# Kernel tuning notes

Hardware: AMD Instinct MI355X
Metric: run time of the kernel (lower is better)

## Reference

```python
import jax, jax.numpy as jnp
import numpy as np


def setup_inputs() -> dict:
    key = jax.random.key(0)
    k1, k2, k3 = jax.random.split(key, 3)
    b, n, h, d = 2, 2048, 16, 64
    q = jax.random.normal(k1, (b, n, h, d), dtype=jnp.float32)
    k = jax.random.normal(k2, (b, n, h, d), dtype=jnp.float32)
    v = jax.random.normal(k3, (b, n, h, d), dtype=jnp.float32)
    return {"q": q, "k": k, "v": v, "is_causal": 1}


def reference(q, k, v, is_causal):
    # q, k, v: [b, n, h, d]
    b, n, h, d = q.shape
    scale = 1.0 / jnp.sqrt(jnp.asarray(d, dtype=q.dtype))
    # scores: [b, h, n_q, n_k]
    scores = jnp.einsum("bqhd,bkhd->bhqk", q, k) * scale
    if is_causal:
        causal_mask = jnp.triu(jnp.ones((n, n), dtype=bool), k=1)  # True above diagonal
        scores = jnp.where(causal_mask[None, None, :, :], jnp.asarray(-jnp.inf, scores.dtype), scores)
    attn = jax.nn.softmax(scores, axis=-1)
    # output back to [b, n, h, d]
    out = jnp.einsum("bhqk,bkhd->bqhd", attn, v)
    return out
```

## Files before the change

kernel.cpp:

```cpp
#include <hip/hip_runtime.h>
#include <hip/hip_bf16.h>
#include <math.h>

typedef __bf16 bf16x8 __attribute__((ext_vector_type(8)));
typedef __bf16 bf16x4 __attribute__((ext_vector_type(4)));
typedef float  f32x4  __attribute__((ext_vector_type(4)));

#define HD  64
#define NQT 32
#define LDK 72
#define LDV 68
#define LDP 72

__global__ __launch_bounds__(256, 4)
void fattn_fwd(const float* __restrict__ Q, const float* __restrict__ K,
               const float* __restrict__ V, const int* __restrict__ causal_p,
               float* __restrict__ O, int B, int N, int H) {
  __shared__ alignas(16) __bf16 Kl[64][LDK];
  __shared__ alignas(16) __bf16 Vl[64][LDV];
  __shared__ alignas(16) __bf16 Pl[64][LDP];

  const int tid  = threadIdx.x;
  const int wave = tid >> 6;
  const int lane = tid & 63;
  const int lo = lane & 15, hi = lane >> 4;

  const int x  = (NQT - 1) - (blockIdx.x >> 5);
  const int bh = blockIdx.x & 31;
  const int bb = bh / H, hh = bh - bb * H;

  const int causal = causal_p[0];
  const int sN = H * HD;

  const float* Qb = Q + (long)bb * N * sN + hh * HD;
  const float* Kb = K + (long)bb * N * sN + hh * HD;
  const float* Vb = V + (long)bb * N * sN + hh * HD;
  float*       Ob = O + (long)bb * N * sN + hh * HD;

  const int q0 = x * 64;
  const int ntile = causal ? (x + 1) : NQT;

  const float qscale = 0.125f * 1.44269504088896340736f;
  bf16x8 aq[2];
  {
    const float* qp = Qb + (long)(q0 + wave * 16 + lo) * sN;
#pragma unroll
    for (int c = 0; c < 2; ++c) {
      f32x4 x0 = *(const f32x4*)(qp + c * 32 + hi * 8);
      f32x4 x1 = *(const f32x4*)(qp + c * 32 + hi * 8 + 4);
      bf16x8 a;
#pragma unroll
      for (int j = 0; j < 4; ++j) {
        a[j]     = (__bf16)(x0[j] * qscale);
        a[j + 4] = (__bf16)(x1[j] * qscale);
      }
      aq[c] = a;
    }
  }

  f32x4 acc[4];
  float m_run[4], l_run[4];
#pragma unroll
  for (int i = 0; i < 4; ++i) {
    acc[i] = (f32x4){0.f, 0.f, 0.f, 0.f};
    m_run[i] = -INFINITY;
    l_run[i] = 0.f;
  }

  f32x4 kreg[4], vreg[4];
  auto issue = [&](int tt) {
    const int k0 = tt * 64;
#pragma unroll
    for (int i = 0; i < 4; ++i) {
      const int fl = tid + i * 256;
      const int r = fl >> 4, c4 = (fl & 15) * 4;
      kreg[i] = *(const f32x4*)(Kb + (long)(k0 + r) * sN + c4);
    }
    const float* vrow = Vb + (long)(k0 + wave * 16 + hi * 4) * sN + lo * 4;
#pragma unroll
    for (int q = 0; q < 4; ++q) vreg[q] = *(const f32x4*)(vrow + (long)q * sN);
  };
  auto wr = [&]() {
#pragma unroll
    for (int i = 0; i < 4; ++i) {
      const int fl = tid + i * 256;
      const int r = fl >> 4, c4 = (fl & 15) * 4;
      bf16x4 kb;
#pragma unroll
      for (int j = 0; j < 4; ++j) kb[j] = (__bf16)kreg[i][j];
      *(bf16x4*)&Kl[r][c4] = kb;
    }
#pragma unroll
    for (int j = 0; j < 4; ++j) {
      bf16x4 vv;
#pragma unroll
      for (int q = 0; q < 4; ++q) vv[q] = (__bf16)vreg[q][j];
      *(bf16x4*)&Vl[lo * 4 + j][wave * 16 + hi * 4] = vv;
    }
  };

  issue(0);
  wr();
  __syncthreads();

  for (int t = 0; t < ntile; ++t) {
    const bool pf = (t + 1 < ntile);
    if (pf) issue(t + 1);
    const int k0 = t * 64;

    f32x4 s[4];
#pragma unroll
    for (int nt = 0; nt < 4; ++nt) s[nt] = (f32x4){0.f, 0.f, 0.f, 0.f};
#pragma unroll
    for (int c = 0; c < 2; ++c) {
#pragma unroll
      for (int nt = 0; nt < 4; ++nt) {
        bf16x8 b = *(const bf16x8*)&Kl[nt * 16 + lo][c * 32 + hi * 8];
        s[nt] = __builtin_amdgcn_mfma_f32_16x16x32_bf16(aq[c], b, s[nt], 0, 0, 0);
      }
    }

    if (causal && t == x) {
#pragma unroll
      for (int nt = 0; nt < 4; ++nt) {
        const int kvg = k0 + nt * 16 + lo;
#pragma unroll
        for (int r = 0; r < 4; ++r) {
          const int qg = q0 + wave * 16 + hi * 4 + r;
          if (kvg > qg) s[nt][r] = -INFINITY;
        }
      }
    }

#pragma unroll
    for (int r = 0; r < 4; ++r) {
      float mx = fmaxf(fmaxf(s[0][r], s[1][r]), fmaxf(s[2][r], s[3][r]));
      mx = fmaxf(mx, __shfl_xor(mx, 1));
      mx = fmaxf(mx, __shfl_xor(mx, 2));
      mx = fmaxf(mx, __shfl_xor(mx, 4));
      mx = fmaxf(mx, __shfl_xor(mx, 8));
      const float mnew = fmaxf(m_run[r], mx);
      const float fac  = exp2f(m_run[r] - mnew);
      float ps = 0.f;
#pragma unroll
      for (int nt = 0; nt < 4; ++nt) {
        const float p = exp2f(s[nt][r] - mnew);
        s[nt][r] = p;
        ps += p;
      }
      ps += __shfl_xor(ps, 1);
      ps += __shfl_xor(ps, 2);
      ps += __shfl_xor(ps, 4);
      ps += __shfl_xor(ps, 8);
      l_run[r] = l_run[r] * fac + ps;
      m_run[r] = mnew;
#pragma unroll
      for (int nt = 0; nt < 4; ++nt) acc[nt][r] *= fac;
    }

    asm volatile("s_waitcnt lgkmcnt(0)" ::: "memory");
#pragma unroll
    for (int nt = 0; nt < 4; ++nt)
#pragma unroll
      for (int r = 0; r < 4; ++r)
        Pl[wave * 16 + hi * 4 + r][nt * 16 + lo] = (__bf16)s[nt][r];
    asm volatile("s_waitcnt lgkmcnt(0)" ::: "memory");

#pragma unroll
    for (int c = 0; c < 2; ++c) {
      bf16x8 pa = *(const bf16x8*)&Pl[wave * 16 + lo][c * 32 + hi * 8];
#pragma unroll
      for (int nt = 0; nt < 4; ++nt) {
        const __bf16* vp = &Vl[nt * 16 + lo][c * 32 + hi * 8];
        bf16x4 v0 = *(const bf16x4*)vp;
        bf16x4 v1 = *(const bf16x4*)(vp + 4);
        bf16x8 vb;
#pragma unroll
        for (int j = 0; j < 4; ++j) { vb[j] = v0[j]; vb[j + 4] = v1[j]; }
        acc[nt] = __builtin_amdgcn_mfma_f32_16x16x32_bf16(pa, vb, acc[nt], 0, 0, 0);
      }
    }

    __syncthreads();
    if (pf) wr();
    __syncthreads();
  }

  {
    const int qrow = q0 + wave * 16 + hi * 4;
#pragma unroll
    for (int nt = 0; nt < 4; ++nt) {
#pragma unroll
      for (int r = 0; r < 4; ++r) {
        Ob[(long)(qrow + r) * sN + nt * 16 + lo] = acc[nt][r] / l_run[r];
      }
    }
  }
}

extern "C" void kernel_launch(void* const* d_in, const int* in_sizes, int n_in,
                              void* d_out, int out_size, void* d_ws, size_t ws_size,
                              hipStream_t stream) {
  const float* q = (const float*)d_in[0];
  const float* k = (const float*)d_in[1];
  const float* v = (const float*)d_in[2];
  const int* causal = (const int*)d_in[3];
  float* out = (float*)d_out;
  const int B = 2, N = 2048, H = 16;
  dim3 grid(NQT * B * H);
  fattn_fwd<<<grid, dim3(256), 0, stream>>>(q, k, v, causal, out, B, N, H);
}
```

Baseline: 159.7 us.

## Switch to 32x32 MFMA with register-resident P and swizzled LDS tiles

Moves to 128-query blocks where each wave owns 32 queries and uses 32x32x16 bf16 MFMAs with a transposed formulation (S^T = K·Q^T, O^T = V^T·P^T). The softmax probabilities are repacked in registers with cross-half shuffles instead of going through an LDS P buffer. K and V tiles are XOR-swizzled in LDS to avoid bank conflicts, and output stores are vectorised. The aim is to cut LDS traffic and synchronisation per tile and raise MFMA efficiency. The cost is higher register pressure (launch bounds drop to 2), half as many blocks, and coarser causal load balance.

```diff
diff --git a/kernel.cpp b/kernel.cpp
--- a/kernel.cpp
+++ b/kernel.cpp
@@ -4,28 +4,38 @@
 
 typedef __bf16 bf16x8 __attribute__((ext_vector_type(8)));
 typedef __bf16 bf16x4 __attribute__((ext_vector_type(4)));
+typedef __bf16 bf16x2 __attribute__((ext_vector_type(2)));
 typedef float  f32x4  __attribute__((ext_vector_type(4)));
-
-#define HD  64
-#define NQT 32
-#define LDK 72
-#define LDV 68
-#define LDP 72
-
-__global__ __launch_bounds__(256, 4)
+typedef float  f32x16 __attribute__((ext_vector_type(16)));
+typedef unsigned int u32;
+typedef unsigned int u32x4 __attribute__((ext_vector_type(4)));
+
+#define HD   64
+#define NQB  16
+#define MNEG (-1e30f)
+#define KSW(r, c) ((c) ^ (((r) & 7) << 3))
+#define VSW(r, c) ((c) ^ ((((r) >> 2) & 7) << 3))
+
+static __device__ __forceinline__ u32 pkbf(float a, float b) {
+  bf16x2 t; t[0] = (__bf16)a; t[1] = (__bf16)b;
+  return __builtin_bit_cast(u32, t);
+}
+
+__global__ __launch_bounds__(256, 2)
 void fattn_fwd(const float* __restrict__ Q, const float* __restrict__ K,
                const float* __restrict__ V, const int* __restrict__ causal_p,
                float* __restrict__ O, int B, int N, int H) {
-  __shared__ alignas(16) __bf16 Kl[64][LDK];
-  __shared__ alignas(16) __bf16 Vl[64][LDV];
-  __shared__ alignas(16) __bf16 Pl[64][LDP];
+  __shared__ alignas(16) __bf16 Kl[64][64];
+  __shared__ alignas(16) __bf16 Vt[64][64];
 
   const int tid  = threadIdx.x;
   const int wave = tid >> 6;
   const int lane = tid & 63;
-  const int lo = lane & 15, hi = lane >> 4;
-
-  const int x  = (NQT - 1) - (blockIdx.x >> 5);
+  const int l31  = lane & 31;
+  const int h    = lane >> 5;
+  const int lo16 = lane & 15, hi4 = lane >> 4;
+
+  const int x  = (NQB - 1) - ((int)blockIdx.x >> 5);
   const int bh = blockIdx.x & 31;
   const int bb = bh / H, hh = bh - bb * H;
 
@@ -37,35 +47,31 @@
   const float* Vb = V + (long)bb * N * sN + hh * HD;
   float*       Ob = O + (long)bb * N * sN + hh * HD;
 
-  const int q0 = x * 64;
-  const int ntile = causal ? (x + 1) : NQT;
+  const int q0w   = x * 128 + wave * 32;
+  const int ntile = causal ? (2 * x + 2) : (2 * NQB);
 
   const float qscale = 0.125f * 1.44269504088896340736f;
-  bf16x8 aq[2];
+  bf16x8 aq[4];
   {
-    const float* qp = Qb + (long)(q0 + wave * 16 + lo) * sN;
-#pragma unroll
-    for (int c = 0; c < 2; ++c) {
-      f32x4 x0 = *(const f32x4*)(qp + c * 32 + hi * 8);
-      f32x4 x1 = *(const f32x4*)(qp + c * 32 + hi * 8 + 4);
+    const float* qrow = Qb + (long)(q0w + l31) * sN;
+#pragma unroll
+    for (int ds = 0; ds < 4; ++ds) {
+      f32x4 x0 = *(const f32x4*)(qrow + ds * 16 + h * 8);
+      f32x4 x1 = *(const f32x4*)(qrow + ds * 16 + h * 8 + 4);
       bf16x8 a;
 #pragma unroll
       for (int j = 0; j < 4; ++j) {
         a[j]     = (__bf16)(x0[j] * qscale);
         a[j + 4] = (__bf16)(x1[j] * qscale);
       }
-      aq[c] = a;
+      aq[ds] = a;
     }
   }
 
-  f32x4 acc[4];
-  float m_run[4], l_run[4];
-#pragma unroll
-  for (int i = 0; i < 4; ++i) {
-    acc[i] = (f32x4){0.f, 0.f, 0.f, 0.f};
-    m_run[i] = -INFINITY;
-    l_run[i] = 0.f;
-  }
+  f32x16 accA, accB;
+#pragma unroll
+  for (int j = 0; j < 16; ++j) { accA[j] = 0.f; accB[j] = 0.f; }
+  float m_run = MNEG, l_run = 0.f;
 
   f32x4 kreg[4], vreg[4];
   auto issue = [&](int tt) {
@@ -76,7 +82,7 @@
       const int r = fl >> 4, c4 = (fl & 15) * 4;
       kreg[i] = *(const f32x4*)(Kb + (long)(k0 + r) * sN + c4);
     }
-    const float* vrow = Vb + (long)(k0 + wave * 16 + hi * 4) * sN + lo * 4;
+    const float* vrow = Vb + (long)(k0 + wave * 16 + hi4 * 4) * sN + lo16 * 4;
 #pragma unroll
     for (int q = 0; q < 4; ++q) vreg[q] = *(const f32x4*)(vrow + (long)q * sN);
   };
@@ -88,14 +94,16 @@
       bf16x4 kb;
 #pragma unroll
       for (int j = 0; j < 4; ++j) kb[j] = (__bf16)kreg[i][j];
-      *(bf16x4*)&Kl[r][c4] = kb;
-    }
+      *(bf16x4*)&Kl[r][KSW(r, c4)] = kb;
+    }
+    const int kv0 = wave * 16 + hi4 * 4;
 #pragma unroll
     for (int j = 0; j < 4; ++j) {
+      const int d = lo16 * 4 + j;
       bf16x4 vv;
 #pragma unroll
       for (int q = 0; q < 4; ++q) vv[q] = (__bf16)vreg[q][j];
-      *(bf16x4*)&Vl[lo * 4 + j][wave * 16 + hi * 4] = vv;
+      *(bf16x4*)&Vt[d][VSW(d, kv0)] = vv;
     }
   };
 
@@ -108,77 +116,92 @@
     if (pf) issue(t + 1);
     const int k0 = t * 64;
 
-    f32x4 s[4];
-#pragma unroll
-    for (int nt = 0; nt < 4; ++nt) s[nt] = (f32x4){0.f, 0.f, 0.f, 0.f};
-#pragma unroll
-    for (int c = 0; c < 2; ++c) {
-#pragma unroll
-      for (int nt = 0; nt < 4; ++nt) {
-        bf16x8 b = *(const bf16x8*)&Kl[nt * 16 + lo][c * 32 + hi * 8];
-        s[nt] = __builtin_amdgcn_mfma_f32_16x16x32_bf16(aq[c], b, s[nt], 0, 0, 0);
+    f32x16 p0, p1;
+#pragma unroll
+    for (int j = 0; j < 16; ++j) { p0[j] = 0.f; p1[j] = 0.f; }
+#pragma unroll
+    for (int ds = 0; ds < 4; ++ds) {
+      const int cc = ds * 16 + h * 8;
+      bf16x8 ka = *(const bf16x8*)&Kl[l31][KSW(l31, cc)];
+      p0 = __builtin_amdgcn_mfma_f32_32x32x16_bf16(ka, aq[ds], p0, 0, 0, 0);
+      bf16x8 kb2 = *(const bf16x8*)&Kl[32 + l31][KSW(32 + l31, cc)];
+      p1 = __builtin_amdgcn_mfma_f32_32x32x16_bf16(kb2, aq[ds], p1, 0, 0, 0);
+    }
+
+    if (causal && t >= ntile - 2) {
+      const int qg = q0w + l31;
+#pragma unroll
+      for (int reg = 0; reg < 16; ++reg) {
+        const int crow = (reg & 3) + 8 * (reg >> 2) + 4 * h;
+        if (k0 + crow > qg)      p0[reg] = MNEG;
+        if (k0 + 32 + crow > qg) p1[reg] = MNEG;
       }
     }
 
-    if (causal && t == x) {
-#pragma unroll
-      for (int nt = 0; nt < 4; ++nt) {
-        const int kvg = k0 + nt * 16 + lo;
-#pragma unroll
-        for (int r = 0; r < 4; ++r) {
-          const int qg = q0 + wave * 16 + hi * 4 + r;
-          if (kvg > qg) s[nt][r] = -INFINITY;
-        }
-      }
-    }
-
-#pragma unroll
-    for (int r = 0; r < 4; ++r) {
-      float mx = fmaxf(fmaxf(s[0][r], s[1][r]), fmaxf(s[2][r], s[3][r]));
-      mx = fmaxf(mx, __shfl_xor(mx, 1));
-      mx = fmaxf(mx, __shfl_xor(mx, 2));
-      mx = fmaxf(mx, __shfl_xor(mx, 4));
-      mx = fmaxf(mx, __shfl_xor(mx, 8));
-      const float mnew = fmaxf(m_run[r], mx);
-      const float fac  = exp2f(m_run[r] - mnew);
-      float ps = 0.f;
-#pragma unroll
-      for (int nt = 0; nt < 4; ++nt) {
-        const float p = exp2f(s[nt][r] - mnew);
-        s[nt][r] = p;
-        ps += p;
-      }
-      ps += __shfl_xor(ps, 1);
-      ps += __shfl_xor(ps, 2);
-      ps += __shfl_xor(ps, 4);
-      ps += __shfl_xor(ps, 8);
-      l_run[r] = l_run[r] * fac + ps;
-      m_run[r] = mnew;
-#pragma unroll
-      for (int nt = 0; nt < 4; ++nt) acc[nt][r] *= fac;
-    }
-
-    asm volatile("s_waitcnt lgkmcnt(0)" ::: "memory");
-#pragma unroll
-    for (int nt = 0; nt < 4; ++nt)
-#pragma unroll
-      for (int r = 0; r < 4; ++r)
-        Pl[wave * 16 + hi * 4 + r][nt * 16 + lo] = (__bf16)s[nt][r];
-    asm volatile("s_waitcnt lgkmcnt(0)" ::: "memory");
-
-#pragma unroll
-    for (int c = 0; c < 2; ++c) {
-      bf16x8 pa = *(const bf16x8*)&Pl[wave * 16 + lo][c * 32 + hi * 8];
-#pragma unroll
-      for (int nt = 0; nt < 4; ++nt) {
-        const __bf16* vp = &Vl[nt * 16 + lo][c * 32 + hi * 8];
-        bf16x4 v0 = *(const bf16x4*)vp;
-        bf16x4 v1 = *(const bf16x4*)(vp + 4);
-        bf16x8 vb;
-#pragma unroll
-        for (int j = 0; j < 4; ++j) { vb[j] = v0[j]; vb[j + 4] = v1[j]; }
-        acc[nt] = __builtin_amdgcn_mfma_f32_16x16x32_bf16(pa, vb, acc[nt], 0, 0, 0);
-      }
+    float t8[8];
+#pragma unroll
+    for (int j = 0; j < 8; ++j)
+      t8[j] = fmaxf(fmaxf(p0[j], p0[j + 8]), fmaxf(p1[j], p1[j + 8]));
+#pragma unroll
+    for (int stp = 4; stp > 0; stp >>= 1)
+#pragma unroll
+      for (int j = 0; j < stp; ++j) t8[j] = fmaxf(t8[j], t8[j + stp]);
+    const float mx = fmaxf(t8[0], __shfl_xor(t8[0], 32));
+    const float mnew = fmaxf(m_run, mx);
+    const float fac  = exp2f(m_run - mnew);
+#pragma unroll
+    for (int j = 0; j < 16; ++j) {
+      p0[j] = exp2f(p0[j] - mnew);
+      p1[j] = exp2f(p1[j] - mnew);
+    }
+    float s8[8];
+#pragma unroll
+    for (int j = 0; j < 8; ++j)
+      s8[j] = (p0[j] + p0[j + 8]) + (p1[j] + p1[j + 8]);
+#pragma unroll
+    for (int stp = 4; stp > 0; stp >>= 1)
+#pragma unroll
+      for (int j = 0; j < stp; ++j) s8[j] += s8[j + stp];
+    const float ps = s8[0] + __shfl_xor(s8[0], 32);
+    l_run = l_run * fac + ps;
+    m_run = mnew;
+#pragma unroll
+    for (int j = 0; j < 16; ++j) { accA[j] *= fac; accB[j] *= fac; }
+
+    u32 W0[8], W1[8];
+#pragma unroll
+    for (int tt = 0; tt < 8; ++tt) {
+      W0[tt] = pkbf(p0[2 * tt], p0[2 * tt + 1]);
+      W1[tt] = pkbf(p1[2 * tt], p1[2 * tt + 1]);
+    }
+    auto mkpair = [&](u32 wa, u32 wb, u32& dlo, u32& dhi) {
+      const u32 gsel = h ? wa : wb;
+      const u32 f = (u32)__shfl_xor((int)gsel, 32);
+      dlo = h ? f : wa;
+      dhi = h ? wb : f;
+    };
+    bf16x8 pa[4];
+    {
+      u32 d0, d1, d2, d3;
+      mkpair(W0[0], W0[2], d0, d2); mkpair(W0[1], W0[3], d1, d3);
+      pa[0] = __builtin_bit_cast(bf16x8, (u32x4){d0, d1, d2, d3});
+      mkpair(W0[4], W0[6], d0, d2); mkpair(W0[5], W0[7], d1, d3);
+      pa[1] = __builtin_bit_cast(bf16x8, (u32x4){d0, d1, d2, d3});
+      mkpair(W1[0], W1[2], d0, d2); mkpair(W1[1], W1[3], d1, d3);
+      pa[2] = __builtin_bit_cast(bf16x8, (u32x4){d0, d1, d2, d3});
+      mkpair(W1[4], W1[6], d0, d2); mkpair(W1[5], W1[7], d1, d3);
+      pa[3] = __builtin_bit_cast(bf16x8, (u32x4){d0, d1, d2, d3});
+    }
+
+#pragma unroll
+    for (int ks = 0; ks < 4; ++ks) {
+      bf16x8 va = *(const bf16x8*)&Vt[l31][VSW(l31, ks * 16 + h * 8)];
+      accA = __builtin_amdgcn_mfma_f32_32x32x16_bf16(va, pa[ks], accA, 0, 0, 0);
+    }
+#pragma unroll
+    for (int ks = 0; ks < 4; ++ks) {
+      bf16x8 va = *(const bf16x8*)&Vt[32 + l31][VSW(32 + l31, ks * 16 + h * 8)];
+      accB = __builtin_amdgcn_mfma_f32_32x32x16_bf16(va, pa[ks], accB, 0, 0, 0);
     }
 
     __syncthreads();
@@ -187,13 +210,18 @@
   }
 
   {
-    const int qrow = q0 + wave * 16 + hi * 4;
-#pragma unroll
-    for (int nt = 0; nt < 4; ++nt) {
-#pragma unroll
-      for (int r = 0; r < 4; ++r) {
-        Ob[(long)(qrow + r) * sN + nt * 16 + lo] = acc[nt][r] / l_run[r];
+    const float linv = 1.0f / l_run;
+    float* orow = Ob + (long)(q0w + l31) * sN;
+#pragma unroll
+    for (int g = 0; g < 4; ++g) {
+      f32x4 o0, o1;
+#pragma unroll
+      for (int j = 0; j < 4; ++j) {
+        o0[j] = accA[4 * g + j] * linv;
+        o1[j] = accB[4 * g + j] * linv;
       }
+      *(f32x4*)(orow + 8 * g + 4 * h) = o0;
+      *(f32x4*)(orow + 32 + 8 * g + 4 * h) = o1;
     }
   }
 }
@@ -207,6 +235,6 @@
   const int* causal = (const int*)d_in[3];
   float* out = (float*)d_out;
   const int B = 2, N = 2048, H = 16;
-  dim3 grid(NQT * B * H);
+  dim3 grid(NQB * B * H);
   fattn_fwd<<<grid, dim3(256), 0, stream>>>(q, k, v, causal, out, B, N, H);
 }
```

Result: faster. 142.6 us (-10.7%).
